# Kernel tuning notes

Hardware: AMD Instinct MI355X
Metric: run time of the kernel (lower is better)

## Reference

```python
import jax, jax.numpy as jnp
import numpy as np


def setup_inputs() -> dict:
    key = jax.random.key(0)
    ks = jax.random.split(key, 5)
    B, N, Fin, Fout = 8, 2048, 512, 512
    stdv = 1.0 / np.sqrt(Fout)
    w_stdv = 1.0 / np.sqrt(Fin)
    x = jax.random.normal(ks[0], (B, N, Fin), dtype=jnp.float32)
    weight = jax.random.uniform(ks[1], (Fin, Fout), dtype=jnp.float32, minval=-stdv, maxval=stdv)
    bias = jax.random.uniform(ks[2], (Fout,), dtype=jnp.float32, minval=-stdv, maxval=stdv)
    w_one = jax.random.uniform(ks[3], (Fin, Fin), dtype=jnp.float32, minval=-w_stdv, maxval=w_stdv)
    w_two = jax.random.uniform(ks[4], (Fin, Fin), dtype=jnp.float32, minval=-w_stdv, maxval=w_stdv)
    return {"x": x, "weight": weight, "bias": bias, "w_one": w_one, "w_two": w_two}


def reference(x, weight, bias, w_one, w_two):
    # x: [B, N, Fin]
    support = jnp.einsum('bnf,fo->bno', x, weight)          # [B, N, Fout]
    phi_one = jnp.einsum('ef,bnf->ben', w_one, x)           # [B, Fin, N]
    phi_two = jnp.einsum('ef,bnf->ben', w_two, x)           # [B, Fin, N]
    adj = jnp.einsum('ben,bem->bnm', phi_one, phi_two)      # [B, N, N]
    adj = jax.nn.softmax(adj, axis=1)                        # softmax over dim=1 (columns)
    out = jnp.einsum('bnm,bmo->bno', adj, support)           # [B, N, Fout]
    return out + bias
```

## Files before the change

### kernel.cpp

```cpp
#include <hip/hip_runtime.h>
#include <math.h>

#define BB 8
#define NN 2048
#define FF 512
#define LOG2E 1.4426950408889634f

typedef __attribute__((ext_vector_type(8))) short short8;
typedef __attribute__((ext_vector_type(4))) float floatx4;
typedef __attribute__((ext_vector_type(2))) float float2v;
typedef __attribute__((ext_vector_type(2))) __bf16 bf16x2;

__device__ __forceinline__ unsigned short f2bf(float f) {
    union { float f; unsigned u; } v; v.f = f;
    unsigned r = v.u + 0x7FFFu + ((v.u >> 16) & 1u);
    return (unsigned short)(r >> 16);
}

__device__ __forceinline__ float fexp2(float x) {
#if __has_builtin(__builtin_amdgcn_exp2f)
    return __builtin_amdgcn_exp2f(x);
#else
    return __expf(x * 0.69314718056f);
#endif
}

__device__ __forceinline__ void pk_store(unsigned short* p0, unsigned short* p1,
                                         float a, float b) {
    union { bf16x2 h; unsigned short s[2]; } u;
    float2v v; v.x = a; v.y = b;
    u.h = __builtin_convertvector(v, bf16x2);
    *p0 = u.s[0]; *p1 = u.s[1];
}

#define BARRIER() do { __builtin_amdgcn_sched_barrier(0); \
                       __builtin_amdgcn_s_barrier(); \
                       __builtin_amdgcn_sched_barrier(0); } while (0)

template<int M_REP, int MODE>
__global__ __launch_bounds__(512, 2) void gemm8p(
    const unsigned short* __restrict__ A, const unsigned short* __restrict__ B,
    void* __restrict__ Cv, const float* __restrict__ bias, float* __restrict__ Dsum,
    int K, int a_ld, int b_ld, int ldc,
    long a_batch, long b_batch, long c_batch)
{
    constexpr int BM  = M_REP * 32;
    constexpr int LA  = BM / 128;
    constexpr int VMS = 2 * LA + 2;

    __shared__ __align__(16) unsigned short Ah[2][2][BM * 32];
    __shared__ __align__(16) unsigned short Bh[2][2][256 * 32];

    const int tid  = threadIdx.x;
    const int wave = tid >> 6;
    const int lane = tid & 63;
    const int wr   = wave >> 2;
    const int wc   = wave & 3;
    const int fl   = lane & 15;
    const int quad = lane >> 4;
    const int bz   = blockIdx.z;

    const int m0 = blockIdx.y * BM;
    const int n0 = blockIdx.x * 256;

    const unsigned short* Aptr = A + (long)bz * a_batch + (long)m0 * a_ld;
    const unsigned short* Bptr = B + (long)bz * b_batch + (long)n0 * b_ld;

    int offA[LA], offB[2];
    #pragma unroll
    for (int i = 0; i < LA; ++i) {
        const int cl = i * 512 + tid;
        const int r = cl >> 2, s = cl & 3;
        offA[i] = r * a_ld + (s ^ ((r >> 1) & 3)) * 8;
    }
    #pragma unroll
    for (int i = 0; i < 2; ++i) {
        const int cl = i * 512 + tid;
        const int r = cl >> 2, s = cl & 3;
        offB[i] = r * b_ld + (s ^ ((r >> 1) & 3)) * 8;
    }

    const int swz = (quad ^ ((fl >> 1) & 3)) * 8;
    const int aRd = (wr * (M_REP * 16) + fl) * 32 + swz;
    const int bRd = (wc * 64 + fl) * 32 + swz;

    auto stageA = [&](int kh, int db, int kbase) {
        #pragma unroll
        for (int i = 0; i < LA; ++i)
            __builtin_amdgcn_global_load_lds(
                (const __attribute__((address_space(1))) void*)(Aptr + kbase + offA[i]),
                (__attribute__((address_space(3))) void*)&Ah[kh][db][(i * 512 + tid) * 8],
                16, 0, 0);
    };
    auto stageB = [&](int kh, int db, int kbase) {
        #pragma unroll
        for (int i = 0; i < 2; ++i)
            __builtin_amdgcn_global_load_lds(
                (const __attribute__((address_space(1))) void*)(Bptr + kbase + offB[i]),
                (__attribute__((address_space(3))) void*)&Bh[kh][db][(i * 512 + tid) * 8],
                16, 0, 0);
    };

    floatx4 acc[M_REP][4] = {};
    short8 af[M_REP];
    short8 bf[2];

    auto LOADA = [&](int kh, int db) {
        const unsigned short* base = &Ah[kh][db][aRd];
        #pragma unroll
        for (int m = 0; m < M_REP; ++m)
            af[m] = *(const short8*)(base + m * 512);
    };
    auto LOADB = [&](int kh, int db, int nh) {
        const unsigned short* base = &Bh[kh][db][bRd + nh * 1024];
        bf[0] = *(const short8*)(base);
        bf[1] = *(const short8*)(base + 512);
    };
    auto MFMAQ = [&](int nh) {
        __builtin_amdgcn_s_setprio(1);
        #pragma unroll
        for (int m = 0; m < M_REP; ++m) {
            acc[m][nh * 2]     = __builtin_amdgcn_mfma_f32_16x16x32_bf16(af[m], bf[0], acc[m][nh * 2], 0, 0, 0);
            acc[m][nh * 2 + 1] = __builtin_amdgcn_mfma_f32_16x16x32_bf16(af[m], bf[1], acc[m][nh * 2 + 1], 0, 0, 0);
        }
        __builtin_amdgcn_s_setprio(0);
    };

    const int nt = K >> 6;
    const int ni = nt >> 1;

    stageA(0, 0, 0);  stageB(0, 0, 0);  stageA(1, 0, 32);  stageB(1, 0, 32);
    stageA(0, 1, 64); stageB(0, 1, 64); stageA(1, 1, 96);
    if constexpr (VMS == 6) asm volatile("s_waitcnt vmcnt(6)" ::: "memory");
    else                    asm volatile("s_waitcnt vmcnt(4)" ::: "memory");
    BARRIER();

    for (int i = 0; i < ni; ++i) {
        const bool last = (i == ni - 1);
        const int kb1 = (2 * i + 1) * 64;
        const int kb2 = (2 * i + 2) * 64;
        const int kb3 = (2 * i + 3) * 64;

        LOADA(0, 0); LOADB(0, 0, 0);
        stageB(1, 1, kb1 + 32);
        BARRIER(); MFMAQ(0); BARRIER();

        LOADB(0, 0, 1);
        if (!last) stageA(0, 0, kb2);
        BARRIER(); MFMAQ(1); BARRIER();

        LOADA(1, 0); LOADB(1, 0, 0);
        if (!last) stageB(0, 0, kb2);
        BARRIER(); MFMAQ(0); BARRIER();

        LOADB(1, 0, 1);
        if (!last) {
            stageA(1, 0, kb2 + 32);
            if constexpr (VMS == 6) asm volatile("s_waitcnt vmcnt(6)" ::: "memory");
            else                    asm volatile("s_waitcnt vmcnt(4)" ::: "memory");
        } else {
            asm volatile("s_waitcnt vmcnt(0)" ::: "memory");
        }
        BARRIER(); MFMAQ(1); BARRIER();

        LOADA(0, 1); LOADB(0, 1, 0);
        if (!last) stageB(1, 0, kb2 + 32);
        BARRIER(); MFMAQ(0); BARRIER();

        LOADB(0, 1, 1);
        if (!last) stageA(0, 1, kb3);
        BARRIER(); MFMAQ(1); BARRIER();

        LOADA(1, 1); LOADB(1, 1, 0);
        if (!last) stageB(0, 1, kb3);
        BARRIER(); MFMAQ(0); BARRIER();

        LOADB(1, 1, 1);
        if (!last) {
            stageA(1, 1, kb3 + 32);
            if constexpr (VMS == 6) asm volatile("s_waitcnt vmcnt(6)" ::: "memory");
            else                    asm volatile("s_waitcnt vmcnt(4)" ::: "memory");
        }
        BARRIER(); MFMAQ(1); BARRIER();
    }

    const int wmg = m0 + wr * (M_REP * 16);
    const int wng = n0 + wc * 64;

    if constexpr (MODE == 0) {
        float* Cb = (float*)Cv + (long)bz * c_batch;
        #pragma unroll
        for (int n = 0; n < 4; ++n) {
            const int ng = wng + n * 16 + fl;
            const float badd = bias ? bias[ng] : 0.0f;
            #pragma unroll
            for (int m = 0; m < M_REP; ++m) {
                const int mg = wmg + m * 16 + quad * 4;
                #pragma unroll
                for (int r = 0; r < 4; ++r)
                    Cb[(long)(mg + r) * ldc + ng] = acc[m][n][r] + badd;
            }
        }
    } else if constexpr (MODE == 1) {
        unsigned short* Cb = (unsigned short*)Cv + (long)bz * c_batch;
        #pragma unroll
        for (int n = 0; n < 4; ++n) {
            const int ng = wng + n * 16 + fl;
            #pragma unroll
            for (int m = 0; m < M_REP; ++m) {
                const int mg = wmg + m * 16 + quad * 4;
                pk_store(&Cb[(long)(mg + 0) * ldc + ng], &Cb[(long)(mg + 1) * ldc + ng],
                         acc[m][n][0], acc[m][n][1]);
                pk_store(&Cb[(long)(mg + 2) * ldc + ng], &Cb[(long)(mg + 3) * ldc + ng],
                         acc[m][n][2], acc[m][n][3]);
            }
        }
    } else {
        unsigned short* Cb = (unsigned short*)Cv + (long)bz * c_batch;
        float* Db = Dsum + (long)bz * NN;
        #pragma unroll
        for (int m = 0; m < M_REP; ++m)
            #pragma unroll
            for (int n = 0; n < 4; ++n)
                #pragma unroll
                for (int r = 0; r < 4; ++r)
                    acc[m][n][r] = fexp2(acc[m][n][r]);
        #pragma unroll
        for (int n = 0; n < 4; ++n) {
            const int ng = wng + n * 16 + fl;
            float csum = 0.f;
            #pragma unroll
            for (int m = 0; m < M_REP; ++m) {
                const int mg = wmg + m * 16 + quad * 4;
                csum += acc[m][n][0] + acc[m][n][1] + acc[m][n][2] + acc[m][n][3];
                pk_store(&Cb[(long)(mg + 0) * ldc + ng], &Cb[(long)(mg + 1) * ldc + ng],
                         acc[m][n][0], acc[m][n][1]);
                pk_store(&Cb[(long)(mg + 2) * ldc + ng], &Cb[(long)(mg + 3) * ldc + ng],
                         acc[m][n][2], acc[m][n][3]);
            }
            csum += __shfl_xor(csum, 16);
            csum += __shfl_xor(csum, 32);
            if (quad == 0) atomicAdd(&Db[ng], csum);
        }
    }
}

__global__ __launch_bounds__(256) void convert_all(
    const float* __restrict__ x, const float* __restrict__ w1, const float* __restrict__ w2,
    unsigned short* __restrict__ xb, unsigned short* __restrict__ w1b, unsigned short* __restrict__ w2b)
{
    const long NX = (long)BB * NN * FF / 8;
    const long NW = (long)FF * FF / 8;
    long t = (long)blockIdx.x * 256 + threadIdx.x;
    const float* in; unsigned short* out; float sc = 1.0f;
    if (t < NX) { in = x; out = xb; }
    else if (t < NX + NW) { in = w1; out = w1b; t -= NX; sc = LOG2E; }
    else if (t < NX + 2 * NW) { in = w2; out = w2b; t -= NX + NW; }
    else return;
    const long i = t * 8;
    float4 a = *(const float4*)(in + i);
    float4 b = *(const float4*)(in + i + 4);
    union { bf16x2 h[4]; short8 s8; } u;
    float2v v;
    v.x = a.x * sc; v.y = a.y * sc; u.h[0] = __builtin_convertvector(v, bf16x2);
    v.x = a.z * sc; v.y = a.w * sc; u.h[1] = __builtin_convertvector(v, bf16x2);
    v.x = b.x * sc; v.y = b.y * sc; u.h[2] = __builtin_convertvector(v, bf16x2);
    v.x = b.z * sc; v.y = b.w * sc; u.h[3] = __builtin_convertvector(v, bf16x2);
    *(short8*)(out + i) = u.s8;
}

__global__ __launch_bounds__(256) void transpose_convert(
    const float* __restrict__ in, unsigned short* __restrict__ out, int dim)
{
    __shared__ float t[32][33];
    const int tx = threadIdx.x & 31, ty = threadIdx.x >> 5;
    const int x0 = blockIdx.x * 32, y0 = blockIdx.y * 32;
    #pragma unroll
    for (int k = 0; k < 32; k += 8)
        t[ty + k][tx] = in[(long)(y0 + ty + k) * dim + x0 + tx];
    __syncthreads();
    #pragma unroll
    for (int k = 0; k < 32; k += 8)
        out[(long)(x0 + ty + k) * dim + y0 + tx] = f2bf(t[tx][ty + k]);
}

__global__ __launch_bounds__(256) void zero_f32(float* __restrict__ p, long n)
{
    long i = (long)blockIdx.x * 256 + threadIdx.x;
    if (i < n) p[i] = 0.0f;
}

__global__ __launch_bounds__(256) void scale_transpose(
    const unsigned short* __restrict__ Call, const float* __restrict__ D,
    unsigned short* __restrict__ supT, int batch0)
{
    __shared__ float t[32][33];
    __shared__ float rD[32];
    const int tx = threadIdx.x & 31, ty = threadIdx.x >> 5;
    const int mt = blockIdx.x * 32, ot = blockIdx.y * 32;
    const int b = batch0 + blockIdx.z;
    const unsigned short* Cb = Call + (long)b * NN * 1536;
    unsigned short* Tb = supT + (long)b * NN * FF;
    if (threadIdx.x < 32) rD[threadIdx.x] = 1.0f / D[(long)b * NN + mt + threadIdx.x];
    __syncthreads();
    #pragma unroll
    for (int k = 0; k < 32; k += 8) {
        unsigned short u = Cb[(long)(mt + ty + k) * 1536 + 1024 + ot + tx];
        union { unsigned uu; float f; } cv; cv.uu = ((unsigned)u) << 16;
        t[ty + k][tx] = cv.f;
    }
    __syncthreads();
    #pragma unroll
    for (int k = 0; k < 32; k += 8)
        Tb[(long)(ot + ty + k) * NN + mt + tx] = f2bf(t[tx][ty + k] * rD[tx]);
}

extern "C" void kernel_launch(void* const* d_in, const int* in_sizes, int n_in,
                              void* d_out, int out_size, void* d_ws, size_t ws_size,
                              hipStream_t stream)
{
    const float* x      = (const float*)d_in[0];
    const float* weight = (const float*)d_in[1];
    const float* bias   = (const float*)d_in[2];
    const float* w_one  = (const float*)d_in[3];
    const float* w_two  = (const float*)d_in[4];
    float* out = (float*)d_out;

    const long NF  = (long)NN * FF;
    const long NN2 = (long)NN * NN;
    const long CROW = 1536;

    char* p = (char*)d_ws;
    unsigned short* xb    = (unsigned short*)p; p += (size_t)BB * NF * 2;
    unsigned short* Wall  = (unsigned short*)p; p += (size_t)CROW * FF * 2;
    unsigned short* Call  = (unsigned short*)p; p += (size_t)BB * NN * CROW * 2;
    unsigned short* supT  = (unsigned short*)p; p += (size_t)BB * NF * 2;
    float*          Dsum  = (float*)p;          p += (size_t)BB * NN * 4;
    unsigned short* E     = (unsigned short*)p;
    unsigned short* w1b = Wall;
    unsigned short* w2b = Wall + (size_t)FF * FF;
    unsigned short* wTb = Wall + (size_t)2 * FF * FF;

    const size_t fixed = (size_t)(p - (char*)d_ws);
    const bool full = ws_size >= fixed + (size_t)BB * NN2 * 2;

    dim3 blk(256), blk5(512);

    convert_all<<<dim3(4352), blk, 0, stream>>>(x, w_one, w_two, xb, w1b, w2b);
    transpose_convert<<<dim3(FF / 32, FF / 32), blk, 0, stream>>>(weight, wTb, FF);
    zero_f32<<<dim3((BB * NN) / 256), blk, 0, stream>>>(Dsum, BB * NN);

    gemm8p<4, 1><<<dim3(CROW / 256, NN / 128, BB), blk5, 0, stream>>>(
        xb, Wall, Call, nullptr, nullptr, FF,
        FF, FF, (int)CROW, NF, 0, NN * CROW);

    if (full) {
        gemm8p<8, 2><<<dim3(NN / 256, NN / 256, BB), blk5, 0, stream>>>(
            Call, Call + FF, E, nullptr, Dsum, FF,
            (int)CROW, (int)CROW, NN, NN * CROW, NN * CROW, NN2);
        scale_transpose<<<dim3(NN / 32, FF / 32, BB), blk, 0, stream>>>(Call, Dsum, supT, 0);
        gemm8p<4, 0><<<dim3(FF / 256, NN / 128, BB), blk5, 0, stream>>>(
            E, supT, out, bias, nullptr, NN,
            NN, NN, FF, NN2, NF, NF);
    } else {
        for (int b = 0; b < BB; ++b) {
            const unsigned short* Cb = Call + (size_t)b * NN * CROW;
            gemm8p<8, 2><<<dim3(NN / 256, NN / 256, 1), blk5, 0, stream>>>(
                Cb, Cb + FF, E, nullptr, Dsum + (size_t)b * NN, FF,
                (int)CROW, (int)CROW, NN, 0, 0, 0);
            scale_transpose<<<dim3(NN / 32, FF / 32, 1), blk, 0, stream>>>(Call, Dsum, supT, b);
            gemm8p<4, 0><<<dim3(FF / 256, NN / 128, 1), blk5, 0, stream>>>(
                E, supT + (size_t)b * NF, out + (size_t)b * NF, bias, nullptr, NN,
                NN, NN, FF, 0, 0, 0);
        }
    }
}
```

Baseline: 249.2 us.

## Restructure GEMM to 4 waves with larger per-wave tiles, register double-buffering and LDS-staged stores

The GEMM kernel moves from 8 waves (512 threads) to 4 waves (256 threads). Each wave now computes a 128-column slab with 8 accumulator tiles, so each A fragment is reused across more MFMAs and fewer LDS reads are issued per MFMA. LDS fragment loads are double-buffered in registers (afA/afB, bfA/bfB) so the next reads overlap the current MFMA batch. Blocks are remapped with an XCD-aware swizzle, and the bf16 output modes stage results through LDS so global stores are coalesced 16-byte writes. The trade-off is higher register pressure and occupancy of one block per CU, plus twice the global-to-LDS loads per thread.

```diff
diff --git a/kernel.cpp b/kernel.cpp
--- a/kernel.cpp
+++ b/kernel.cpp
@@ -25,173 +25,177 @@
 #endif
 }
 
-__device__ __forceinline__ void pk_store(unsigned short* p0, unsigned short* p1,
-                                         float a, float b) {
-    union { bf16x2 h; unsigned short s[2]; } u;
-    float2v v; v.x = a; v.y = b;
-    u.h = __builtin_convertvector(v, bf16x2);
-    *p0 = u.s[0]; *p1 = u.s[1];
-}
-
-#define BARRIER() do { __builtin_amdgcn_sched_barrier(0); \
-                       __builtin_amdgcn_s_barrier(); \
-                       __builtin_amdgcn_sched_barrier(0); } while (0)
+#define SB0() __builtin_amdgcn_sched_barrier(0)
+#define BARRIER() do { SB0(); __builtin_amdgcn_s_barrier(); SB0(); } while (0)
+#define GLDS(src, dst) __builtin_amdgcn_global_load_lds( \
+    (const __attribute__((address_space(1))) void*)(src), \
+    (__attribute__((address_space(3))) void*)(dst), 16, 0, 0)
+#define VMW(n) asm volatile("s_waitcnt vmcnt(" #n ")" ::: "memory")
 
 template<int M_REP, int MODE>
-__global__ __launch_bounds__(512, 2) void gemm8p(
+__global__ __launch_bounds__(256, 1) void gemm8p(
     const unsigned short* __restrict__ A, const unsigned short* __restrict__ B,
     void* __restrict__ Cv, const float* __restrict__ bias, float* __restrict__ Dsum,
     int K, int a_ld, int b_ld, int ldc,
     long a_batch, long b_batch, long c_batch)
 {
-    constexpr int BM  = M_REP * 32;
-    constexpr int LA  = BM / 128;
-    constexpr int VMS = 2 * LA + 2;
-
-    __shared__ __align__(16) unsigned short Ah[2][2][BM * 32];
-    __shared__ __align__(16) unsigned short Bh[2][2][256 * 32];
+    constexpr int BM    = M_REP * 32;
+    constexpr int LA    = BM / 64;
+    constexpr int ASLOT = BM * 32;
+    constexpr int BSLOT = 256 * 32;
+    constexpr int BBASE = 4 * ASLOT;
+    constexpr int TOT   = 4 * ASLOT + 4 * BSLOT;
+
+    __shared__ __align__(16) unsigned short SH[TOT];
 
     const int tid  = threadIdx.x;
     const int wave = tid >> 6;
     const int lane = tid & 63;
-    const int wr   = wave >> 2;
-    const int wc   = wave & 3;
+    const int wr   = wave >> 1;
+    const int wc   = wave & 1;
     const int fl   = lane & 15;
     const int quad = lane >> 4;
-    const int bz   = blockIdx.z;
-
-    const int m0 = blockIdx.y * BM;
-    const int n0 = blockIdx.x * 256;
+
+    const int gx = gridDim.x, gy = gridDim.y;
+    int flat = blockIdx.x + gx * (blockIdx.y + gy * blockIdx.z);
+    const int cpx = (gx * gy * gridDim.z) >> 3;
+    flat = (flat & 7) * cpx + (flat >> 3);
+    const int bx = flat % gx;
+    const int rest = flat / gx;
+    const int by = rest % gy;
+    const int bz = rest / gy;
+
+    const int m0 = by * BM;
+    const int n0 = bx * 256;
 
     const unsigned short* Aptr = A + (long)bz * a_batch + (long)m0 * a_ld;
     const unsigned short* Bptr = B + (long)bz * b_batch + (long)n0 * b_ld;
 
-    int offA[LA], offB[2];
+    int offA[LA], offB[4];
     #pragma unroll
     for (int i = 0; i < LA; ++i) {
-        const int cl = i * 512 + tid;
+        const int cl = i * 256 + tid;
         const int r = cl >> 2, s = cl & 3;
         offA[i] = r * a_ld + (s ^ ((r >> 1) & 3)) * 8;
     }
     #pragma unroll
-    for (int i = 0; i < 2; ++i) {
-        const int cl = i * 512 + tid;
+    for (int i = 0; i < 4; ++i) {
+        const int cl = i * 256 + tid;
         const int r = cl >> 2, s = cl & 3;
         offB[i] = r * b_ld + (s ^ ((r >> 1) & 3)) * 8;
     }
 
     const int swz = (quad ^ ((fl >> 1) & 3)) * 8;
     const int aRd = (wr * (M_REP * 16) + fl) * 32 + swz;
-    const int bRd = (wc * 64 + fl) * 32 + swz;
-
-    auto stageA = [&](int kh, int db, int kbase) {
+    const int bRd = (wc * 128 + fl) * 32 + swz;
+
+    auto sA = [&](int kh, int db, int kb) {
         #pragma unroll
         for (int i = 0; i < LA; ++i)
-            __builtin_amdgcn_global_load_lds(
-                (const __attribute__((address_space(1))) void*)(Aptr + kbase + offA[i]),
-                (__attribute__((address_space(3))) void*)&Ah[kh][db][(i * 512 + tid) * 8],
-                16, 0, 0);
-    };
-    auto stageB = [&](int kh, int db, int kbase) {
-        #pragma unroll
-        for (int i = 0; i < 2; ++i)
-            __builtin_amdgcn_global_load_lds(
-                (const __attribute__((address_space(1))) void*)(Bptr + kbase + offB[i]),
-                (__attribute__((address_space(3))) void*)&Bh[kh][db][(i * 512 + tid) * 8],
-                16, 0, 0);
-    };
-
-    floatx4 acc[M_REP][4] = {};
-    short8 af[M_REP];
-    short8 bf[2];
-
-    auto LOADA = [&](int kh, int db) {
-        const unsigned short* base = &Ah[kh][db][aRd];
+            GLDS(Aptr + kb + offA[i], &SH[(kh * 2 + db) * ASLOT + (i * 256 + tid) * 8]);
+    };
+    auto sB = [&](int kh, int db, int kb) {
+        #pragma unroll
+        for (int i = 0; i < 4; ++i)
+            GLDS(Bptr + kb + offB[i], &SH[BBASE + (kh * 2 + db) * BSLOT + (i * 256 + tid) * 8]);
+    };
+
+    floatx4 acc[M_REP][8] = {};
+    short8 afA[M_REP], afB[M_REP], bfA[4], bfB[4];
+
+    auto RA = [&](short8* af, int kh, int db) {
+        const unsigned short* b = &SH[(kh * 2 + db) * ASLOT + aRd];
+        #pragma unroll
+        for (int m = 0; m < M_REP; ++m) af[m] = *(const short8*)(b + m * 512);
+    };
+    auto RB = [&](short8* bf, int kh, int db, int nh) {
+        const unsigned short* b = &SH[BBASE + (kh * 2 + db) * BSLOT + bRd + nh * 2048];
+        #pragma unroll
+        for (int j = 0; j < 4; ++j) bf[j] = *(const short8*)(b + j * 512);
+    };
+    auto MC = [&](short8* af, short8* bf, int nh) {
+        __builtin_amdgcn_s_setprio(1);
         #pragma unroll
         for (int m = 0; m < M_REP; ++m)
-            af[m] = *(const short8*)(base + m * 512);
-    };
-    auto LOADB = [&](int kh, int db, int nh) {
-        const unsigned short* base = &Bh[kh][db][bRd + nh * 1024];
-        bf[0] = *(const short8*)(base);
-        bf[1] = *(const short8*)(base + 512);
-    };
-    auto MFMAQ = [&](int nh) {
-        __builtin_amdgcn_s_setprio(1);
-        #pragma unroll
-        for (int m = 0; m < M_REP; ++m) {
-            acc[m][nh * 2]     = __builtin_amdgcn_mfma_f32_16x16x32_bf16(af[m], bf[0], acc[m][nh * 2], 0, 0, 0);
-            acc[m][nh * 2 + 1] = __builtin_amdgcn_mfma_f32_16x16x32_bf16(af[m], bf[1], acc[m][nh * 2 + 1], 0, 0, 0);
-        }
+            #pragma unroll
+            for (int j = 0; j < 4; ++j)
+                acc[m][nh * 4 + j] = __builtin_amdgcn_mfma_f32_16x16x32_bf16(af[m], bf[j], acc[m][nh * 4 + j], 0, 0, 0);
         __builtin_amdgcn_s_setprio(0);
     };
 
     const int nt = K >> 6;
     const int ni = nt >> 1;
 
-    stageA(0, 0, 0);  stageB(0, 0, 0);  stageA(1, 0, 32);  stageB(1, 0, 32);
-    stageA(0, 1, 64); stageB(0, 1, 64); stageA(1, 1, 96);
-    if constexpr (VMS == 6) asm volatile("s_waitcnt vmcnt(6)" ::: "memory");
-    else                    asm volatile("s_waitcnt vmcnt(4)" ::: "memory");
+    sA(0, 0, 0);  sB(0, 0, 0);  sA(1, 0, 32); sB(1, 0, 32);
+    sA(0, 1, 64); sB(0, 1, 64); sA(1, 1, 96);
+    if constexpr (M_REP == 8) VMW(12); else VMW(8);
     BARRIER();
+    RA(afA, 0, 0); RB(bfA, 0, 0, 0);
+    SB0();
 
     for (int i = 0; i < ni; ++i) {
         const bool last = (i == ni - 1);
-        const int kb1 = (2 * i + 1) * 64;
-        const int kb2 = (2 * i + 2) * 64;
-        const int kb3 = (2 * i + 3) * 64;
-
-        LOADA(0, 0); LOADB(0, 0, 0);
-        stageB(1, 1, kb1 + 32);
-        BARRIER(); MFMAQ(0); BARRIER();
-
-        LOADB(0, 0, 1);
-        if (!last) stageA(0, 0, kb2);
-        BARRIER(); MFMAQ(1); BARRIER();
-
-        LOADA(1, 0); LOADB(1, 0, 0);
-        if (!last) stageB(0, 0, kb2);
-        BARRIER(); MFMAQ(0); BARRIER();
-
-        LOADB(1, 0, 1);
+        const int kb1 = (2 * i + 1) * 64, kb2 = kb1 + 64, kb3 = kb2 + 64;
+
+        sB(1, 1, kb1 + 32);
+        BARRIER();
+        RB(bfB, 0, 0, 1); SB0();
+        MC(afA, bfA, 0);
+        BARRIER();
+        if (!last) sA(0, 0, kb2);
+        BARRIER();
+        RA(afB, 1, 0); RB(bfA, 1, 0, 0); SB0();
+        MC(afA, bfB, 1);
+        BARRIER();
+        if (!last) sB(0, 0, kb2);
+        BARRIER();
+        RB(bfB, 1, 0, 1); SB0();
+        MC(afB, bfA, 0);
+        BARRIER();
         if (!last) {
-            stageA(1, 0, kb2 + 32);
-            if constexpr (VMS == 6) asm volatile("s_waitcnt vmcnt(6)" ::: "memory");
-            else                    asm volatile("s_waitcnt vmcnt(4)" ::: "memory");
+            sA(1, 0, kb2 + 32);
+            if constexpr (M_REP == 8) VMW(12); else VMW(8);
         } else {
-            asm volatile("s_waitcnt vmcnt(0)" ::: "memory");
-        }
-        BARRIER(); MFMAQ(1); BARRIER();
-
-        LOADA(0, 1); LOADB(0, 1, 0);
-        if (!last) stageB(1, 0, kb2 + 32);
-        BARRIER(); MFMAQ(0); BARRIER();
-
-        LOADB(0, 1, 1);
-        if (!last) stageA(0, 1, kb3);
-        BARRIER(); MFMAQ(1); BARRIER();
-
-        LOADA(1, 1); LOADB(1, 1, 0);
-        if (!last) stageB(0, 1, kb3);
-        BARRIER(); MFMAQ(0); BARRIER();
-
-        LOADB(1, 1, 1);
+            VMW(0);
+        }
+        BARRIER();
+        RA(afA, 0, 1); RB(bfA, 0, 1, 0); SB0();
+        MC(afB, bfB, 1);
+        BARRIER();
+        if (!last) sB(1, 0, kb2 + 32);
+        BARRIER();
+        RB(bfB, 0, 1, 1); SB0();
+        MC(afA, bfA, 0);
+        BARRIER();
+        if (!last) sA(0, 1, kb3);
+        BARRIER();
+        RA(afB, 1, 1); RB(bfA, 1, 1, 0); SB0();
+        MC(afA, bfB, 1);
+        BARRIER();
+        if (!last) sB(0, 1, kb3);
+        BARRIER();
+        RB(bfB, 1, 1, 1); SB0();
+        MC(afB, bfA, 0);
+        BARRIER();
         if (!last) {
-            stageA(1, 1, kb3 + 32);
-            if constexpr (VMS == 6) asm volatile("s_waitcnt vmcnt(6)" ::: "memory");
-            else                    asm volatile("s_waitcnt vmcnt(4)" ::: "memory");
-        }
-        BARRIER(); MFMAQ(1); BARRIER();
+            sA(1, 1, kb3 + 32);
+            if constexpr (M_REP == 8) VMW(12); else VMW(8);
+        }
+        BARRIER();
+        if (!last) { RA(afA, 0, 0); RB(bfA, 0, 0, 0); }
+        SB0();
+        MC(afB, bfB, 1);
+        BARRIER();
     }
 
     const int wmg = m0 + wr * (M_REP * 16);
-    const int wng = n0 + wc * 64;
+    const int wcol = wc * 128;
 
     if constexpr (MODE == 0) {
         float* Cb = (float*)Cv + (long)bz * c_batch;
         #pragma unroll
-        for (int n = 0; n < 4; ++n) {
-            const int ng = wng + n * 16 + fl;
+        for (int n = 0; n < 8; ++n) {
+            const int ng = n0 + wcol + n * 16 + fl;
             const float badd = bias ? bias[ng] : 0.0f;
             #pragma unroll
             for (int m = 0; m < M_REP; ++m) {
@@ -201,46 +205,47 @@
                     Cb[(long)(mg + r) * ldc + ng] = acc[m][n][r] + badd;
             }
         }
-    } else if constexpr (MODE == 1) {
-        unsigned short* Cb = (unsigned short*)Cv + (long)bz * c_batch;
-        #pragma unroll
-        for (int n = 0; n < 4; ++n) {
-            const int ng = wng + n * 16 + fl;
-            #pragma unroll
-            for (int m = 0; m < M_REP; ++m) {
-                const int mg = wmg + m * 16 + quad * 4;
-                pk_store(&Cb[(long)(mg + 0) * ldc + ng], &Cb[(long)(mg + 1) * ldc + ng],
-                         acc[m][n][0], acc[m][n][1]);
-                pk_store(&Cb[(long)(mg + 2) * ldc + ng], &Cb[(long)(mg + 3) * ldc + ng],
-                         acc[m][n][2], acc[m][n][3]);
-            }
-        }
     } else {
         unsigned short* Cb = (unsigned short*)Cv + (long)bz * c_batch;
-        float* Db = Dsum + (long)bz * NN;
-        #pragma unroll
-        for (int m = 0; m < M_REP; ++m)
-            #pragma unroll
-            for (int n = 0; n < 4; ++n)
+        if constexpr (MODE == 2) {
+            float* Db = Dsum + (long)bz * NN;
+            #pragma unroll
+            for (int m = 0; m < M_REP; ++m)
+                #pragma unroll
+                for (int n = 0; n < 8; ++n)
+                    #pragma unroll
+                    for (int r = 0; r < 4; ++r)
+                        acc[m][n][r] = fexp2(acc[m][n][r]);
+            #pragma unroll
+            for (int n = 0; n < 8; ++n) {
+                float csum = 0.f;
+                #pragma unroll
+                for (int m = 0; m < M_REP; ++m)
+                    csum += acc[m][n][0] + acc[m][n][1] + acc[m][n][2] + acc[m][n][3];
+                csum += __shfl_xor(csum, 16);
+                csum += __shfl_xor(csum, 32);
+                if (quad == 0) atomicAdd(&Db[n0 + wcol + n * 16 + fl], csum);
+            }
+        }
+        #pragma unroll
+        for (int m = 0; m < M_REP; ++m) {
+            const int rowb = wr * (M_REP * 16) + m * 16 + quad * 4;
+            #pragma unroll
+            for (int n = 0; n < 8; ++n) {
+                const int pc = (wcol + n * 16 + fl) ^ (quad << 4);
                 #pragma unroll
                 for (int r = 0; r < 4; ++r)
-                    acc[m][n][r] = fexp2(acc[m][n][r]);
-        #pragma unroll
-        for (int n = 0; n < 4; ++n) {
-            const int ng = wng + n * 16 + fl;
-            float csum = 0.f;
-            #pragma unroll
-            for (int m = 0; m < M_REP; ++m) {
-                const int mg = wmg + m * 16 + quad * 4;
-                csum += acc[m][n][0] + acc[m][n][1] + acc[m][n][2] + acc[m][n][3];
-                pk_store(&Cb[(long)(mg + 0) * ldc + ng], &Cb[(long)(mg + 1) * ldc + ng],
-                         acc[m][n][0], acc[m][n][1]);
-                pk_store(&Cb[(long)(mg + 2) * ldc + ng], &Cb[(long)(mg + 3) * ldc + ng],
-                         acc[m][n][2], acc[m][n][3]);
+                    SH[(rowb + r) * 256 + pc] = f2bf(acc[m][n][r]);
             }
-            csum += __shfl_xor(csum, 16);
-            csum += __shfl_xor(csum, 32);
-            if (quad == 0) atomicAdd(&Db[ng], csum);
+        }
+        __syncthreads();
+        #pragma unroll
+        for (int k = 0; k < BM / 8; ++k) {
+            const int idx = k * 256 + tid;
+            const int row = idx >> 5, c8 = (idx & 31) * 8;
+            const int lcol = c8 ^ (((row >> 2) & 3) << 4);
+            short8 vv = *(const short8*)&SH[row * 256 + lcol];
+            *(short8*)&Cb[(long)(m0 + row) * ldc + n0 + c8] = vv;
         }
     }
 }
@@ -344,32 +349,32 @@
     const size_t fixed = (size_t)(p - (char*)d_ws);
     const bool full = ws_size >= fixed + (size_t)BB * NN2 * 2;
 
-    dim3 blk(256), blk5(512);
+    dim3 blk(256);
 
     convert_all<<<dim3(4352), blk, 0, stream>>>(x, w_one, w_two, xb, w1b, w2b);
     transpose_convert<<<dim3(FF / 32, FF / 32), blk, 0, stream>>>(weight, wTb, FF);
     zero_f32<<<dim3((BB * NN) / 256), blk, 0, stream>>>(Dsum, BB * NN);
 
-    gemm8p<4, 1><<<dim3(CROW / 256, NN / 128, BB), blk5, 0, stream>>>(
+    gemm8p<4, 1><<<dim3(CROW / 256, NN / 128, BB), blk, 0, stream>>>(
         xb, Wall, Call, nullptr, nullptr, FF,
         FF, FF, (int)CROW, NF, 0, NN * CROW);
 
     if (full) {
-        gemm8p<8, 2><<<dim3(NN / 256, NN / 256, BB), blk5, 0, stream>>>(
+        gemm8p<8, 2><<<dim3(NN / 256, NN / 256, BB), blk, 0, stream>>>(
             Call, Call + FF, E, nullptr, Dsum, FF,
             (int)CROW, (int)CROW, NN, NN * CROW, NN * CROW, NN2);
         scale_transpose<<<dim3(NN / 32, FF / 32, BB), blk, 0, stream>>>(Call, Dsum, supT, 0);
-        gemm8p<4, 0><<<dim3(FF / 256, NN / 128, BB), blk5, 0, stream>>>(
+        gemm8p<4, 0><<<dim3(FF / 256, NN / 128, BB), blk, 0, stream>>>(
             E, supT, out, bias, nullptr, NN,
             NN, NN, FF, NN2, NF, NF);
     } else {
         for (int b = 0; b < BB; ++b) {
             const unsigned short* Cb = Call + (size_t)b * NN * CROW;
-            gemm8p<8, 2><<<dim3(NN / 256, NN / 256, 1), blk5, 0, stream>>>(
+            gemm8p<8, 2><<<dim3(NN / 256, NN / 256, 1), blk, 0, stream>>>(
                 Cb, Cb + FF, E, nullptr, Dsum + (size_t)b * NN, FF,
                 (int)CROW, (int)CROW, NN, 0, 0, 0);
             scale_transpose<<<dim3(NN / 32, FF / 32, 1), blk, 0, stream>>>(Call, Dsum, supT, b);
-            gemm8p<4, 0><<<dim3(FF / 256, NN / 128, 1), blk5, 0, stream>>>(
+            gemm8p<4, 0><<<dim3(FF / 256, NN / 128, 1), blk, 0, stream>>>(
                 E, supT + (size_t)b * NF, out + (size_t)b * NF, bias, nullptr, NN,
                 NN, NN, FF, 0, 0, 0);
         }
```

After: 248.0 us. No clear change (-0.5%).
